# Kernel tuning notes

Measured on AMD Instinct MI355X. Metric: run time of the kernel, lower is better.

## Reference

```python
import jax, jax.numpy as jnp
import numpy as np

N_NODES = 100000


def _spmm(edge_index, edge_weight, x):
    # out[i] = sum_j A[i, j] * x[j]; row=dst=edge_index[0], col=src=edge_index[1]
    dst, src = edge_index[0], edge_index[1]
    msgs = edge_weight[:, None] * x[src]  # [E, d]
    return jax.ops.segment_sum(msgs, dst, num_segments=N_NODES)


def setup_inputs() -> dict:
    key = jax.random.key(0)
    k1, k2, k3, k4 = jax.random.split(key, 4)
    N, E, D = N_NODES, 3200000, 64
    features = jax.random.normal(k1, (N, D), dtype=jnp.float32)
    edge_weight = jax.random.uniform(k2, (E,), dtype=jnp.float32)
    dst = jax.random.randint(k3, (E,), 0, N)
    src = jax.random.randint(k4, (E,), 0, N)
    edge_index = jnp.stack([dst, src]).astype(jnp.int64)
    return {"features": features, "edge_weight": edge_weight,
            "edge_index": edge_index, "degree": 2}


def reference(features, edge_weight, edge_index, degree):
    # SGC: features = adj @ features, repeated `degree` times (no learned params)
    x = features
    for _ in range(degree):
        x = _spmm(edge_index, edge_weight, x)
    return x
```

## Files before the change

### kernel.cpp

```cpp
#include <hip/hip_runtime.h>
#include <hip/hip_fp16.h>

#define N_NODES 100000
#define DFEAT 64
#define CH 4096
#define NBK 391
#define NPB 256

__global__ __launch_bounds__(512) void sort_chunks(
    const int* __restrict__ dst, const int* __restrict__ src,
    const float* __restrict__ w,
    unsigned* __restrict__ recs_g, unsigned char* __restrict__ dloc_g,
    int* __restrict__ off_g, int E)
{
    __shared__ int  hist[NBK + 1];
    __shared__ int  cursor[NBK];
    __shared__ int  sb[512];
    __shared__ unsigned      lrec[CH];
    __shared__ unsigned char ldl[CH];

    const int chunk = blockIdx.x;
    const int base  = chunk * CH;
    const int n     = min(CH, E - base);
    const int tid   = threadIdx.x;

    for (int i = tid; i < NBK + 1; i += 512) hist[i] = 0;
    __syncthreads();

    for (int k = tid; k < n; k += 512) atomicAdd(&hist[dst[base + k] >> 8], 1);
    __syncthreads();

    int v = (tid < NBK) ? hist[tid] : 0;
    sb[tid] = v;
    __syncthreads();
    for (int o = 1; o < 512; o <<= 1) {
        int t = (tid >= o) ? sb[tid - o] : 0;
        __syncthreads();
        sb[tid] += t;
        __syncthreads();
    }
    int excl = sb[tid] - v;
    if (tid <= NBK) {
        off_g[chunk * (NBK + 1) + tid] = base + excl;
        if (tid < NBK) cursor[tid] = excl;
    }
    __syncthreads();

    for (int k = tid; k < n; k += 512) {
        int d = dst[base + k];
        int pos = atomicAdd(&cursor[d >> 8], 1);
        unsigned wq = (unsigned)__float2int_rn(w[base + k] * 32768.0f);
        if (wq > 32767u) wq = 32767u;
        lrec[pos] = (unsigned)src[base + k] | (wq << 17);
        ldl[pos]  = (unsigned char)(d & 255);
    }
    __syncthreads();

    int4* rg = (int4*)(recs_g + base);
    const int4* rl = (const int4*)lrec;
    for (int k = tid; k < ((n + 3) >> 2); k += 512) rg[k] = rl[k];
    int4* dg = (int4*)(dloc_g + base);
    const int4* dl4 = (const int4*)ldl;
    for (int k = tid; k < ((n + 15) >> 4); k += 512) dg[k] = dl4[k];
}

__global__ __launch_bounds__(64) void bucket_tot(
    const int* __restrict__ off_g, int* __restrict__ gtot, int nch)
{
    const int b = blockIdx.x;
    const int lane = threadIdx.x;
    int s = 0;
    for (int c = lane; c < nch; c += 64)
        s += off_g[c * (NBK + 1) + b + 1] - off_g[c * (NBK + 1) + b];
    for (int o = 32; o > 0; o >>= 1) s += __shfl_down(s, o, 64);
    if (lane == 0) gtot[b] = s;
}

__global__ __launch_bounds__(512) void bucket_scan(
    const int* __restrict__ gtot, int* __restrict__ gbase)
{
    __shared__ int sb[512];
    const int tid = threadIdx.x;
    int v = (tid < NBK) ? gtot[tid] : 0;
    sb[tid] = v;
    __syncthreads();
    for (int o = 1; o < 512; o <<= 1) {
        int t = (tid >= o) ? sb[tid - o] : 0;
        __syncthreads();
        sb[tid] += t;
        __syncthreads();
    }
    if (tid < NBK) gbase[tid] = sb[tid] - v;
}

__global__ __launch_bounds__(512) void build_csr(
    const int* __restrict__ off_g, const unsigned* __restrict__ recs_g,
    const unsigned char* __restrict__ dloc_g, const int* __restrict__ gbase,
    unsigned* __restrict__ edges_s, int* __restrict__ row_ptr, int nch)
{
    __shared__ int hist[NPB];
    __shared__ int cursor[NPB];
    __shared__ int sb[512];

    const int b    = blockIdx.x;
    const int tid  = threadIdx.x;
    const int grp  = tid >> 4;
    const int gl   = tid & 15;
    const int gb   = gbase[b];

    if (tid < NPB) hist[tid] = 0;
    __syncthreads();

    for (int c = grp; c < nch; c += 32) {
        int beg = off_g[c * (NBK + 1) + b];
        int end = off_g[c * (NBK + 1) + b + 1];
        for (int k = beg + gl; k < end; k += 16)
            atomicAdd(&hist[dloc_g[k]], 1);
    }
    __syncthreads();

    int v = (tid < NPB) ? hist[tid] : 0;
    sb[tid] = v;
    __syncthreads();
    for (int o = 1; o < 512; o <<= 1) {
        int t = (tid >= o) ? sb[tid - o] : 0;
        __syncthreads();
        sb[tid] += t;
        __syncthreads();
    }
    if (tid < NPB) {
        int excl = sb[tid] - v;
        row_ptr[b * NPB + tid] = gb + excl;
        cursor[tid] = gb + excl;
    }
    if (b == NBK - 1 && tid == 0) row_ptr[NBK * NPB] = gb + sb[NPB - 1];
    __syncthreads();

    for (int c = grp; c < nch; c += 32) {
        int beg = off_g[c * (NBK + 1) + b];
        int end = off_g[c * (NBK + 1) + b + 1];
        for (int k = beg + gl; k < end; k += 16) {
            int pos = atomicAdd(&cursor[dloc_g[k]], 1);
            edges_s[pos] = recs_g[k];
        }
    }
}

__global__ __launch_bounds__(256) void cast_f2h(
    const float* __restrict__ in, __half* __restrict__ out, int n2)
{
    int i = blockIdx.x * blockDim.x + threadIdx.x;
    if (i < n2) {
        float2 f = ((const float2*)in)[i];
        ((__half2*)out)[i] = __floats2half2_rn(f.x, f.y);
    }
}

template <int OUT_FP16>
__global__ __launch_bounds__(256) void spmm_csr(
    const int* __restrict__ row_ptr,
    const unsigned* __restrict__ edges,
    const __half2* __restrict__ x2,
    void* __restrict__ outv)
{
    int node = __builtin_amdgcn_readfirstlane(blockIdx.x * 4 + (int)(threadIdx.x >> 6));
    if (node >= N_NODES) return;
    int lane = threadIdx.x & 63;
    int sub  = lane & 31;
    int half = lane >> 5;

    int beg = row_ptr[node];
    int end = row_ptr[node + 1];

    float ax = 0.f, ay = 0.f;
    int e0 = beg;
    int n16 = (end - beg) >> 4;

    if (n16 > 0) {
        unsigned q[16];
        int eu = __builtin_amdgcn_readfirstlane(e0);
#pragma unroll
        for (int i = 0; i < 16; ++i) q[i] = edges[eu + i];
        e0 += 16;

        for (int blk = 0; blk < n16; ++blk) {
            unsigned s0 = half ? q[1]  : q[0];
            unsigned s1 = half ? q[3]  : q[2];
            unsigned s2 = half ? q[5]  : q[4];
            unsigned s3 = half ? q[7]  : q[6];
            unsigned s4 = half ? q[9]  : q[8];
            unsigned s5 = half ? q[11] : q[10];
            unsigned s6 = half ? q[13] : q[12];
            unsigned s7 = half ? q[15] : q[14];
            __half2 v0 = x2[((size_t)(s0 & 0x1FFFF) << 5) + sub];
            __half2 v1 = x2[((size_t)(s1 & 0x1FFFF) << 5) + sub];
            __half2 v2 = x2[((size_t)(s2 & 0x1FFFF) << 5) + sub];
            __half2 v3 = x2[((size_t)(s3 & 0x1FFFF) << 5) + sub];
            __half2 v4 = x2[((size_t)(s4 & 0x1FFFF) << 5) + sub];
            __half2 v5 = x2[((size_t)(s5 & 0x1FFFF) << 5) + sub];
            __half2 v6 = x2[((size_t)(s6 & 0x1FFFF) << 5) + sub];
            __half2 v7 = x2[((size_t)(s7 & 0x1FFFF) << 5) + sub];
            if (blk + 1 < n16) {
                int eun = __builtin_amdgcn_readfirstlane(e0);
#pragma unroll
                for (int i = 0; i < 16; ++i) q[i] = edges[eun + i];
                e0 += 16;
            }
            float w0 = (float)(s0 >> 17), w1 = (float)(s1 >> 17);
            float w2 = (float)(s2 >> 17), w3 = (float)(s3 >> 17);
            float w4 = (float)(s4 >> 17), w5 = (float)(s5 >> 17);
            float w6 = (float)(s6 >> 17), w7 = (float)(s7 >> 17);
            ax += w0 * __low2float(v0);  ay += w0 * __high2float(v0);
            ax += w1 * __low2float(v1);  ay += w1 * __high2float(v1);
            ax += w2 * __low2float(v2);  ay += w2 * __high2float(v2);
            ax += w3 * __low2float(v3);  ay += w3 * __high2float(v3);
            ax += w4 * __low2float(v4);  ay += w4 * __high2float(v4);
            ax += w5 * __low2float(v5);  ay += w5 * __high2float(v5);
            ax += w6 * __low2float(v6);  ay += w6 * __high2float(v6);
            ax += w7 * __low2float(v7);  ay += w7 * __high2float(v7);
        }
    }

    for (; e0 + 8 <= end; e0 += 8) {
        int eu = __builtin_amdgcn_readfirstlane(e0);
        unsigned q0 = edges[eu],     q1 = edges[eu + 1];
        unsigned q2 = edges[eu + 2], q3 = edges[eu + 3];
        unsigned q4 = edges[eu + 4], q5 = edges[eu + 5];
        unsigned q6 = edges[eu + 6], q7 = edges[eu + 7];
        unsigned s0 = half ? q1 : q0;
        unsigned s1 = half ? q3 : q2;
        unsigned s2 = half ? q5 : q4;
        unsigned s3 = half ? q7 : q6;
        __half2 x0 = x2[((size_t)(s0 & 0x1FFFF) << 5) + sub];
        __half2 x1 = x2[((size_t)(s1 & 0x1FFFF) << 5) + sub];
        __half2 x2v = x2[((size_t)(s2 & 0x1FFFF) << 5) + sub];
        __half2 x3 = x2[((size_t)(s3 & 0x1FFFF) << 5) + sub];
        float w0 = (float)(s0 >> 17), w1 = (float)(s1 >> 17);
        float w2 = (float)(s2 >> 17), w3 = (float)(s3 >> 17);
        ax += w0 * __low2float(x0);  ay += w0 * __high2float(x0);
        ax += w1 * __low2float(x1);  ay += w1 * __high2float(x1);
        ax += w2 * __low2float(x2v); ay += w2 * __high2float(x2v);
        ax += w3 * __low2float(x3);  ay += w3 * __high2float(x3);
    }
    for (; e0 < end; e0 += 2) {
        int e = e0 + half;
        if (e < end) {
            unsigned r = edges[e];
            __half2 xv = x2[((size_t)(r & 0x1FFFF) << 5) + sub];
            float w = (float)(r >> 17);
            ax += w * __low2float(xv);
            ay += w * __high2float(xv);
        }
    }

    ax += __shfl_xor(ax, 32, 64);
    ay += __shfl_xor(ay, 32, 64);

    if (half == 0) {
        float sx = ax * (1.0f / 32768.0f);
        float sy = ay * (1.0f / 32768.0f);
        if (OUT_FP16)
            ((__half2*)outv)[(size_t)node * 32 + sub] = __floats2half2_rn(sx, sy);
        else
            ((float2*)outv)[(size_t)node * 32 + sub] = make_float2(sx, sy);
    }
}

extern "C" void kernel_launch(void* const* d_in, const int* in_sizes, int n_in,
                              void* d_out, int out_size, void* d_ws, size_t ws_size,
                              hipStream_t stream) {
    const float* features = (const float*)d_in[0];
    const float* edge_w   = (const float*)d_in[1];
    const int*   edge_idx = (const int*)d_in[2];

    const int E = in_sizes[1];
    const int* dst = edge_idx;
    const int* src = edge_idx + E;

    const int nch = (E + CH - 1) / CH;

    char* ws = (char*)d_ws;
    unsigned*      recs_g  = (unsigned*)ws;      ws += (size_t)nch * CH * sizeof(unsigned);
    unsigned char* dloc_g  = (unsigned char*)ws; ws += (size_t)nch * CH;
    unsigned*      edges_s = (unsigned*)ws;      ws += (size_t)E * sizeof(unsigned);
    __half*        tmp_h   = (__half*)ws;        ws += (size_t)N_NODES * DFEAT * sizeof(__half);
    int*           off_g   = (int*)ws;           ws += (size_t)nch * (NBK + 1) * sizeof(int);
    int*           row_ptr = (int*)ws;           ws += (size_t)(NBK * NPB + 1) * sizeof(int);
    int*           gtot    = (int*)ws;           ws += (size_t)NBK * sizeof(int);
    int*           gbase   = (int*)ws;           ws += (size_t)NBK * sizeof(int);

    __half* features_h = (__half*)recs_g;

    float* out = (float*)d_out;

    sort_chunks<<<nch, 512, 0, stream>>>(dst, src, edge_w, recs_g, dloc_g, off_g, E);
    bucket_tot<<<NBK, 64, 0, stream>>>(off_g, gtot, nch);
    bucket_scan<<<1, 512, 0, stream>>>(gtot, gbase);
    build_csr<<<NBK, 512, 0, stream>>>(off_g, recs_g, dloc_g, gbase, edges_s, row_ptr, nch);

    const int n2 = N_NODES * DFEAT / 2;
    cast_f2h<<<(n2 + 255) / 256, 256, 0, stream>>>(features, features_h, n2);

    const int ngrid = (N_NODES + 3) / 4;
    spmm_csr<1><<<ngrid, 256, 0, stream>>>(row_ptr, edges_s, (const __half2*)features_h, tmp_h);
    spmm_csr<0><<<ngrid, 256, 0, stream>>>(row_ptr, edges_s, (const __half2*)tmp_h, out);
}
```

Baseline: 287.1 us.

## Replace bucketed chunk sort with global-atomic counting sort for CSR build

```diff
diff --git a/kernel.cpp b/kernel.cpp
--- a/kernel.cpp
+++ b/kernel.cpp
@@ -3,34 +3,48 @@
 
 #define N_NODES 100000
 #define DFEAT 64
-#define CH 4096
-#define NBK 391
-#define NPB 256
-
-__global__ __launch_bounds__(512) void sort_chunks(
-    const int* __restrict__ dst, const int* __restrict__ src,
-    const float* __restrict__ w,
-    unsigned* __restrict__ recs_g, unsigned char* __restrict__ dloc_g,
-    int* __restrict__ off_g, int E)
-{
-    __shared__ int  hist[NBK + 1];
-    __shared__ int  cursor[NBK];
-    __shared__ int  sb[512];
-    __shared__ unsigned      lrec[CH];
-    __shared__ unsigned char ldl[CH];
-
-    const int chunk = blockIdx.x;
-    const int base  = chunk * CH;
-    const int n     = min(CH, E - base);
-    const int tid   = threadIdx.x;
-
-    for (int i = tid; i < NBK + 1; i += 512) hist[i] = 0;
+#define NBLK 391
+
+
+__global__ __launch_bounds__(256) void zero_hist(int* __restrict__ h)
+{
+    int i = blockIdx.x * 256 + threadIdx.x;
+    if (i < N_NODES) h[i] = 0;
+}
+
+__global__ __launch_bounds__(256) void hist_dst(
+    const int* __restrict__ dst, int* __restrict__ hist, int E)
+{
+    int stride = gridDim.x * 256;
+    for (int e = blockIdx.x * 256 + threadIdx.x; e < E; e += stride)
+        atomicAdd(&hist[dst[e]], 1);
+}
+
+__global__ __launch_bounds__(256) void scan_local(
+    const int* __restrict__ hist, int* __restrict__ lexcl, int* __restrict__ gtot)
+{
+    __shared__ int sb[256];
+    const int b = blockIdx.x, t = threadIdx.x;
+    const int i = b * 256 + t;
+    int v = (i < N_NODES) ? hist[i] : 0;
+    sb[t] = v;
     __syncthreads();
-
-    for (int k = tid; k < n; k += 512) atomicAdd(&hist[dst[base + k] >> 8], 1);
-    __syncthreads();
-
-    int v = (tid < NBK) ? hist[tid] : 0;
+    for (int o = 1; o < 256; o <<= 1) {
+        int x = (t >= o) ? sb[t - o] : 0;
+        __syncthreads();
+        sb[t] += x;
+        __syncthreads();
+    }
+    if (i < N_NODES) lexcl[i] = sb[t] - v;
+    if (t == 255) gtot[b] = sb[255];
+}
+
+__global__ __launch_bounds__(512) void block_scan(
+    const int* __restrict__ gtot, int* __restrict__ gbase)
+{
+    __shared__ int sb[512];
+    const int tid = threadIdx.x;
+    int v = (tid < NBLK) ? gtot[tid] : 0;
     sb[tid] = v;
     __syncthreads();
     for (int o = 1; o < 512; o <<= 1) {
@@ -39,110 +53,36 @@
         sb[tid] += t;
         __syncthreads();
     }
-    int excl = sb[tid] - v;
-    if (tid <= NBK) {
-        off_g[chunk * (NBK + 1) + tid] = base + excl;
-        if (tid < NBK) cursor[tid] = excl;
-    }
-    __syncthreads();
-
-    for (int k = tid; k < n; k += 512) {
-        int d = dst[base + k];
-        int pos = atomicAdd(&cursor[d >> 8], 1);
-        unsigned wq = (unsigned)__float2int_rn(w[base + k] * 32768.0f);
+    if (tid < NBLK) gbase[tid] = sb[tid] - v;
+}
+
+__global__ __launch_bounds__(256) void finalize_rp(
+    const int* __restrict__ lexcl, const int* __restrict__ gbase,
+    int* __restrict__ row_ptr, int* __restrict__ cursor, int E)
+{
+    const int b = blockIdx.x, t = threadIdx.x;
+    const int i = b * 256 + t;
+    if (i < N_NODES) {
+        int rp = gbase[b] + lexcl[i];
+        row_ptr[i] = rp;
+        cursor[i]  = rp;
+        if (i == N_NODES - 1) row_ptr[N_NODES] = E;
+    }
+}
+
+__global__ __launch_bounds__(256) void scatter_edges(
+    const int* __restrict__ dst, const int* __restrict__ src,
+    const float* __restrict__ w, int* __restrict__ cursor,
+    unsigned* __restrict__ edges_s, int E)
+{
+    int stride = gridDim.x * 256;
+    for (int e = blockIdx.x * 256 + threadIdx.x; e < E; e += stride) {
+        int d = dst[e];
+        unsigned wq = (unsigned)__float2int_rn(w[e] * 32768.0f);
         if (wq > 32767u) wq = 32767u;
-        lrec[pos] = (unsigned)src[base + k] | (wq << 17);
-        ldl[pos]  = (unsigned char)(d & 255);
-    }
-    __syncthreads();
-
-    int4* rg = (int4*)(recs_g + base);
-    const int4* rl = (const int4*)lrec;
-    for (int k = tid; k < ((n + 3) >> 2); k += 512) rg[k] = rl[k];
-    int4* dg = (int4*)(dloc_g + base);
-    const int4* dl4 = (const int4*)ldl;
-    for (int k = tid; k < ((n + 15) >> 4); k += 512) dg[k] = dl4[k];
-}
-
-__global__ __launch_bounds__(64) void bucket_tot(
-    const int* __restrict__ off_g, int* __restrict__ gtot, int nch)
-{
-    const int b = blockIdx.x;
-    const int lane = threadIdx.x;
-    int s = 0;
-    for (int c = lane; c < nch; c += 64)
-        s += off_g[c * (NBK + 1) + b + 1] - off_g[c * (NBK + 1) + b];
-    for (int o = 32; o > 0; o >>= 1) s += __shfl_down(s, o, 64);
-    if (lane == 0) gtot[b] = s;
-}
-
-__global__ __launch_bounds__(512) void bucket_scan(
-    const int* __restrict__ gtot, int* __restrict__ gbase)
-{
-    __shared__ int sb[512];
-    const int tid = threadIdx.x;
-    int v = (tid < NBK) ? gtot[tid] : 0;
-    sb[tid] = v;
-    __syncthreads();
-    for (int o = 1; o < 512; o <<= 1) {
-        int t = (tid >= o) ? sb[tid - o] : 0;
-        __syncthreads();
-        sb[tid] += t;
-        __syncthreads();
-    }
-    if (tid < NBK) gbase[tid] = sb[tid] - v;
-}
-
-__global__ __launch_bounds__(512) void build_csr(
-    const int* __restrict__ off_g, const unsigned* __restrict__ recs_g,
-    const unsigned char* __restrict__ dloc_g, const int* __restrict__ gbase,
-    unsigned* __restrict__ edges_s, int* __restrict__ row_ptr, int nch)
-{
-    __shared__ int hist[NPB];
-    __shared__ int cursor[NPB];
-    __shared__ int sb[512];
-
-    const int b    = blockIdx.x;
-    const int tid  = threadIdx.x;
-    const int grp  = tid >> 4;
-    const int gl   = tid & 15;
-    const int gb   = gbase[b];
-
-    if (tid < NPB) hist[tid] = 0;
-    __syncthreads();
-
-    for (int c = grp; c < nch; c += 32) {
-        int beg = off_g[c * (NBK + 1) + b];
-        int end = off_g[c * (NBK + 1) + b + 1];
-        for (int k = beg + gl; k < end; k += 16)
-            atomicAdd(&hist[dloc_g[k]], 1);
-    }
-    __syncthreads();
-
-    int v = (tid < NPB) ? hist[tid] : 0;
-    sb[tid] = v;
-    __syncthreads();
-    for (int o = 1; o < 512; o <<= 1) {
-        int t = (tid >= o) ? sb[tid - o] : 0;
-        __syncthreads();
-        sb[tid] += t;
-        __syncthreads();
-    }
-    if (tid < NPB) {
-        int excl = sb[tid] - v;
-        row_ptr[b * NPB + tid] = gb + excl;
-        cursor[tid] = gb + excl;
-    }
-    if (b == NBK - 1 && tid == 0) row_ptr[NBK * NPB] = gb + sb[NPB - 1];
-    __syncthreads();
-
-    for (int c = grp; c < nch; c += 32) {
-        int beg = off_g[c * (NBK + 1) + b];
-        int end = off_g[c * (NBK + 1) + b + 1];
-        for (int k = beg + gl; k < end; k += 16) {
-            int pos = atomicAdd(&cursor[dloc_g[k]], 1);
-            edges_s[pos] = recs_g[k];
-        }
+        unsigned rec = (unsigned)src[e] | (wq << 17);
+        int pos = atomicAdd(&cursor[d], 1);
+        edges_s[pos] = rec;
     }
 }
 
@@ -277,31 +217,30 @@
     const int* dst = edge_idx;
     const int* src = edge_idx + E;
 
-    const int nch = (E + CH - 1) / CH;
-
     char* ws = (char*)d_ws;
-    unsigned*      recs_g  = (unsigned*)ws;      ws += (size_t)nch * CH * sizeof(unsigned);
-    unsigned char* dloc_g  = (unsigned char*)ws; ws += (size_t)nch * CH;
-    unsigned*      edges_s = (unsigned*)ws;      ws += (size_t)E * sizeof(unsigned);
-    __half*        tmp_h   = (__half*)ws;        ws += (size_t)N_NODES * DFEAT * sizeof(__half);
-    int*           off_g   = (int*)ws;           ws += (size_t)nch * (NBK + 1) * sizeof(int);
-    int*           row_ptr = (int*)ws;           ws += (size_t)(NBK * NPB + 1) * sizeof(int);
-    int*           gtot    = (int*)ws;           ws += (size_t)NBK * sizeof(int);
-    int*           gbase   = (int*)ws;           ws += (size_t)NBK * sizeof(int);
-
-    __half* features_h = (__half*)recs_g;
+    unsigned* edges_s = (unsigned*)ws;  ws += (size_t)E * sizeof(unsigned);
+    __half*   tmp_h   = (__half*)ws;    ws += (size_t)N_NODES * DFEAT * sizeof(__half);
+    __half*   feat_h  = (__half*)ws;    ws += (size_t)N_NODES * DFEAT * sizeof(__half);
+    int*      hist    = (int*)ws;       ws += (size_t)N_NODES * sizeof(int);
+    int*      lexcl   = (int*)ws;       ws += (size_t)N_NODES * sizeof(int);
+    int*      cursor  = (int*)ws;       ws += (size_t)N_NODES * sizeof(int);
+    int*      row_ptr = (int*)ws;       ws += (size_t)(N_NODES + 1) * sizeof(int);
+    int*      gtot    = (int*)ws;       ws += (size_t)NBLK * sizeof(int);
+    int*      gbase   = (int*)ws;       ws += (size_t)NBLK * sizeof(int);
 
     float* out = (float*)d_out;
 
-    sort_chunks<<<nch, 512, 0, stream>>>(dst, src, edge_w, recs_g, dloc_g, off_g, E);
-    bucket_tot<<<NBK, 64, 0, stream>>>(off_g, gtot, nch);
-    bucket_scan<<<1, 512, 0, stream>>>(gtot, gbase);
-    build_csr<<<NBK, 512, 0, stream>>>(off_g, recs_g, dloc_g, gbase, edges_s, row_ptr, nch);
+    zero_hist   <<<NBLK, 256, 0, stream>>>(hist);
+    hist_dst    <<<2048, 256, 0, stream>>>(dst, hist, E);
+    scan_local  <<<NBLK, 256, 0, stream>>>(hist, lexcl, gtot);
+    block_scan  <<<1, 512, 0, stream>>>(gtot, gbase);
+    finalize_rp <<<NBLK, 256, 0, stream>>>(lexcl, gbase, row_ptr, cursor, E);
+    scatter_edges<<<2048, 256, 0, stream>>>(dst, src, edge_w, cursor, edges_s, E);
 
     const int n2 = N_NODES * DFEAT / 2;
-    cast_f2h<<<(n2 + 255) / 256, 256, 0, stream>>>(features, features_h, n2);
+    cast_f2h<<<(n2 + 255) / 256, 256, 0, stream>>>(features, feat_h, n2);
 
     const int ngrid = (N_NODES + 3) / 4;
-    spmm_csr<1><<<ngrid, 256, 0, stream>>>(row_ptr, edges_s, (const __half2*)features_h, tmp_h);
+    spmm_csr<1><<<ngrid, 256, 0, stream>>>(row_ptr, edges_s, (const __half2*)feat_h, tmp_h);
     spmm_csr<0><<<ngrid, 256, 0, stream>>>(row_ptr, edges_s, (const __half2*)tmp_h, out);
 }
```

Result: slower. 610.4 us (+112.6%).

## Stage bucket edges in LDS for CSR build and transpose chunk offsets

Applied to the files above, without the earlier changes.

```diff
diff --git a/kernel.cpp b/kernel.cpp
--- a/kernel.cpp
+++ b/kernel.cpp
@@ -3,19 +3,46 @@
 
 #define N_NODES 100000
 #define DFEAT 64
-#define CH 4096
+#define CH 8192
 #define NBK 391
 #define NPB 256
+#define CAPB 9216
+
+__device__ __forceinline__ int block_scan_excl_512(int v, int* sb, int tid, int* total)
+{
+    const int lane = tid & 63, wid = tid >> 6;
+    int inc = v;
+#pragma unroll
+    for (int o = 1; o < 64; o <<= 1) {
+        int t = __shfl_up(inc, o, 64);
+        if (lane >= o) inc += t;
+    }
+    if (lane == 63) sb[wid] = inc;
+    __syncthreads();
+    if (wid == 0) {
+        int wv = (lane < 8) ? sb[lane] : 0;
+        int winc = wv;
+#pragma unroll
+        for (int o = 1; o < 8; o <<= 1) {
+            int t = __shfl_up(winc, o, 64);
+            if (lane >= o) winc += t;
+        }
+        if (lane < 8) sb[8 + lane] = winc - wv;
+    }
+    __syncthreads();
+    *total = sb[15] + sb[7];
+    return sb[8 + wid] + inc - v;
+}
 
 __global__ __launch_bounds__(512) void sort_chunks(
     const int* __restrict__ dst, const int* __restrict__ src,
     const float* __restrict__ w,
     unsigned* __restrict__ recs_g, unsigned char* __restrict__ dloc_g,
-    int* __restrict__ off_g, int E)
+    int* __restrict__ off_T, int E, int nch)
 {
     __shared__ int  hist[NBK + 1];
     __shared__ int  cursor[NBK];
-    __shared__ int  sb[512];
+    __shared__ int  sb[16];
     __shared__ unsigned      lrec[CH];
     __shared__ unsigned char ldl[CH];
 
@@ -24,24 +51,17 @@
     const int n     = min(CH, E - base);
     const int tid   = threadIdx.x;
 
-    for (int i = tid; i < NBK + 1; i += 512) hist[i] = 0;
+    if (tid < NBK + 1) hist[tid] = 0;
     __syncthreads();
 
     for (int k = tid; k < n; k += 512) atomicAdd(&hist[dst[base + k] >> 8], 1);
     __syncthreads();
 
     int v = (tid < NBK) ? hist[tid] : 0;
-    sb[tid] = v;
-    __syncthreads();
-    for (int o = 1; o < 512; o <<= 1) {
-        int t = (tid >= o) ? sb[tid - o] : 0;
-        __syncthreads();
-        sb[tid] += t;
-        __syncthreads();
-    }
-    int excl = sb[tid] - v;
+    int tot;
+    int excl = block_scan_excl_512(v, sb, tid, &tot);
     if (tid <= NBK) {
-        off_g[chunk * (NBK + 1) + tid] = base + excl;
+        off_T[(size_t)tid * nch + chunk] = base + excl;
         if (tid < NBK) cursor[tid] = excl;
     }
     __syncthreads();
@@ -65,13 +85,14 @@
 }
 
 __global__ __launch_bounds__(64) void bucket_tot(
-    const int* __restrict__ off_g, int* __restrict__ gtot, int nch)
+    const int* __restrict__ off_T, int* __restrict__ gtot, int nch)
 {
     const int b = blockIdx.x;
     const int lane = threadIdx.x;
+    const int* r0 = off_T + (size_t)b * nch;
+    const int* r1 = off_T + (size_t)(b + 1) * nch;
     int s = 0;
-    for (int c = lane; c < nch; c += 64)
-        s += off_g[c * (NBK + 1) + b + 1] - off_g[c * (NBK + 1) + b];
+    for (int c = lane; c < nch; c += 64) s += r1[c] - r0[c];
     for (int o = 32; o > 0; o >>= 1) s += __shfl_down(s, o, 64);
     if (lane == 0) gtot[b] = s;
 }
@@ -79,70 +100,74 @@
 __global__ __launch_bounds__(512) void bucket_scan(
     const int* __restrict__ gtot, int* __restrict__ gbase)
 {
-    __shared__ int sb[512];
+    __shared__ int sb[16];
     const int tid = threadIdx.x;
     int v = (tid < NBK) ? gtot[tid] : 0;
-    sb[tid] = v;
-    __syncthreads();
-    for (int o = 1; o < 512; o <<= 1) {
-        int t = (tid >= o) ? sb[tid - o] : 0;
-        __syncthreads();
-        sb[tid] += t;
-        __syncthreads();
-    }
-    if (tid < NBK) gbase[tid] = sb[tid] - v;
+    int tot;
+    int excl = block_scan_excl_512(v, sb, tid, &tot);
+    if (tid < NBK) gbase[tid] = excl;
 }
 
 __global__ __launch_bounds__(512) void build_csr(
-    const int* __restrict__ off_g, const unsigned* __restrict__ recs_g,
+    const int* __restrict__ off_T, const unsigned* __restrict__ recs_g,
     const unsigned char* __restrict__ dloc_g, const int* __restrict__ gbase,
-    unsigned* __restrict__ edges_s, int* __restrict__ row_ptr, int nch)
-{
-    __shared__ int hist[NPB];
-    __shared__ int cursor[NPB];
-    __shared__ int sb[512];
-
-    const int b    = blockIdx.x;
-    const int tid  = threadIdx.x;
-    const int grp  = tid >> 4;
-    const int gl   = tid & 15;
-    const int gb   = gbase[b];
-
-    if (tid < NPB) hist[tid] = 0;
-    __syncthreads();
-
+    unsigned* __restrict__ edges_s, int* __restrict__ row_ptr, int nch, int E)
+{
+    __shared__ unsigned      lrecL[CAPB];
+    __shared__ unsigned char dlocL[CAPB];
+    __shared__ int gsrcL[512];
+    __shared__ int lenL[512];
+    __shared__ int ldstL[512];
+    __shared__ int histL[NPB];
+    __shared__ int cursorL[NPB];
+    __shared__ int sb[16];
+
+    const int b   = blockIdx.x;
+    const int tid = threadIdx.x;
+    const int gb  = gbase[b];
+
+    int len = 0;
+    if (tid < nch) {
+        int a0 = off_T[(size_t)b * nch + tid];
+        int a1 = off_T[(size_t)(b + 1) * nch + tid];
+        gsrcL[tid] = a0;
+        len = a1 - a0;
+        lenL[tid] = len;
+    }
+    int cnt;
+    int dstoff = block_scan_excl_512((tid < nch) ? len : 0, sb, tid, &cnt);
+    if (tid < nch) ldstL[tid] = dstoff;
+    if (tid < NPB) histL[tid] = 0;
+    __syncthreads();
+
+    const int grp = tid >> 4;
+    const int gl  = tid & 15;
     for (int c = grp; c < nch; c += 32) {
-        int beg = off_g[c * (NBK + 1) + b];
-        int end = off_g[c * (NBK + 1) + b + 1];
-        for (int k = beg + gl; k < end; k += 16)
-            atomicAdd(&hist[dloc_g[k]], 1);
-    }
-    __syncthreads();
-
-    int v = (tid < NPB) ? hist[tid] : 0;
-    sb[tid] = v;
-    __syncthreads();
-    for (int o = 1; o < 512; o <<= 1) {
-        int t = (tid >= o) ? sb[tid - o] : 0;
-        __syncthreads();
-        sb[tid] += t;
-        __syncthreads();
-    }
+        int s = gsrcL[c], d = ldstL[c], L = lenL[c];
+        for (int k = gl; k < L; k += 16) {
+            lrecL[d + k] = recs_g[s + k];
+            dlocL[d + k] = dloc_g[s + k];
+        }
+    }
+    __syncthreads();
+
+    for (int k = tid; k < cnt; k += 512) atomicAdd(&histL[dlocL[k]], 1);
+    __syncthreads();
+
+    int hv = (tid < NPB) ? histL[tid] : 0;
+    int htot;
+    int hexcl = block_scan_excl_512(hv, sb, tid, &htot);
     if (tid < NPB) {
-        int excl = sb[tid] - v;
-        row_ptr[b * NPB + tid] = gb + excl;
-        cursor[tid] = gb + excl;
-    }
-    if (b == NBK - 1 && tid == 0) row_ptr[NBK * NPB] = gb + sb[NPB - 1];
-    __syncthreads();
-
-    for (int c = grp; c < nch; c += 32) {
-        int beg = off_g[c * (NBK + 1) + b];
-        int end = off_g[c * (NBK + 1) + b + 1];
-        for (int k = beg + gl; k < end; k += 16) {
-            int pos = atomicAdd(&cursor[dloc_g[k]], 1);
-            edges_s[pos] = recs_g[k];
-        }
+        int i = b * NPB + tid;
+        if (i < N_NODES) row_ptr[i] = gb + hexcl;
+        cursorL[tid] = gb + hexcl;
+    }
+    if (b == NBK - 1 && tid == 0) row_ptr[N_NODES] = E;
+    __syncthreads();
+
+    for (int k = tid; k < cnt; k += 512) {
+        int pos = atomicAdd(&cursorL[dlocL[k]], 1);
+        edges_s[pos] = lrecL[k];
     }
 }
 
@@ -284,8 +309,8 @@
     unsigned char* dloc_g  = (unsigned char*)ws; ws += (size_t)nch * CH;
     unsigned*      edges_s = (unsigned*)ws;      ws += (size_t)E * sizeof(unsigned);
     __half*        tmp_h   = (__half*)ws;        ws += (size_t)N_NODES * DFEAT * sizeof(__half);
-    int*           off_g   = (int*)ws;           ws += (size_t)nch * (NBK + 1) * sizeof(int);
-    int*           row_ptr = (int*)ws;           ws += (size_t)(NBK * NPB + 1) * sizeof(int);
+    int*           off_T   = (int*)ws;           ws += (size_t)(NBK + 1) * nch * sizeof(int);
+    int*           row_ptr = (int*)ws;           ws += (size_t)(N_NODES + 1) * sizeof(int);
     int*           gtot    = (int*)ws;           ws += (size_t)NBK * sizeof(int);
     int*           gbase   = (int*)ws;           ws += (size_t)NBK * sizeof(int);
 
@@ -293,10 +318,10 @@
 
     float* out = (float*)d_out;
 
-    sort_chunks<<<nch, 512, 0, stream>>>(dst, src, edge_w, recs_g, dloc_g, off_g, E);
-    bucket_tot<<<NBK, 64, 0, stream>>>(off_g, gtot, nch);
+    sort_chunks<<<nch, 512, 0, stream>>>(dst, src, edge_w, recs_g, dloc_g, off_T, E, nch);
+    bucket_tot <<<NBK, 64, 0, stream>>>(off_T, gtot, nch);
     bucket_scan<<<1, 512, 0, stream>>>(gtot, gbase);
-    build_csr<<<NBK, 512, 0, stream>>>(off_g, recs_g, dloc_g, gbase, edges_s, row_ptr, nch);
+    build_csr  <<<NBK, 512, 0, stream>>>(off_T, recs_g, dloc_g, gbase, edges_s, row_ptr, nch, E);
 
     const int n2 = N_NODES * DFEAT / 2;
     cast_f2h<<<(n2 + 255) / 256, 256, 0, stream>>>(features, features_h, n2);
```

New measurement: 269.1 us. 1.07x faster.
